# Kernel optimization log

Measured on AMD Instinct MI355X. Metric: run time of the kernel, lower is better.

Reference implementation:

```python
import jax, jax.numpy as jnp
import numpy as np

MASK_VAL = -50000.0
N_HEADS = 16

def setup_inputs() -> dict:
    key = jax.random.key(0)
    k1, k2, k3, k4 = jax.random.split(key, 4)
    b, n, d = 2, 2048, 1024
    s = d ** -0.5  # xavier-ish scale for weights
    return {
        "x": jax.random.normal(k1, (b, n, d), dtype=jnp.float32),
        "Wq": jax.random.normal(k2, (d, d), dtype=jnp.float32) * s,
        "Wkv": jax.random.normal(k3, (d, 2 * d), dtype=jnp.float32) * s,
        "Wo": jax.random.normal(k4, (d, d), dtype=jnp.float32) * s,
    }

def reference(x, Wq, Wkv, Wo):
    b, n, d = x.shape
    h = N_HEADS
    hd = d // h
    scale = hd ** -0.5
    # in-projection
    q = x @ Wq                      # [b, n, d]
    kv = x @ Wkv                    # [b, n, 2d]
    k, v = jnp.split(kv, 2, axis=-1)
    # split heads: b n (h d) -> b h n d
    split = lambda t: t.reshape(b, n, h, hd).transpose(0, 2, 1, 3)
    q, k, v = split(q), split(k), split(v)
    # scaled dot-product scores
    dots = jnp.einsum('bhid,bhjd->bhij', q * scale, k)  # [b, h, n, n]
    # causal mask: upper triangle (j > i) set to MASK_VAL (not -inf, per source)
    causal = jnp.triu(jnp.ones((n, n), dtype=bool), 1)
    dots = jnp.where(causal, MASK_VAL, dots)
    attn = jax.nn.softmax(dots, axis=-1)
    out = jnp.einsum('bhij,bhjd->bhid', attn, v)
    out = out.transpose(0, 2, 1, 3).reshape(b, n, d)  # merge heads
    return out @ Wo
```

## Files before the change

kernel.cpp:

```cpp
#include <hip/hip_runtime.h>
#include <stdint.h>
#include <stddef.h>


typedef __bf16 bf16;
typedef __bf16 bf16x8 __attribute__((ext_vector_type(8)));
typedef __bf16 bf16x4 __attribute__((ext_vector_type(4)));
typedef __bf16 bf16x2 __attribute__((ext_vector_type(2)));
typedef float  f32x4  __attribute__((ext_vector_type(4)));
typedef float  f32x16 __attribute__((ext_vector_type(16)));

#define NSEQ 2048
#define DM   1024
#define HD   64
#define QKVS 3072
#define LOG2E 1.44269504f

#define GLD16(g, l) __builtin_amdgcn_global_load_lds(                         \
    (const __attribute__((address_space(1))) void*)(g),                       \
    (__attribute__((address_space(3))) void*)(l), 16, 0, 0)

__global__ void detect_dtype(const uint32_t* __restrict__ x, int* __restrict__ flag) {
  __shared__ int cnt;
  if (threadIdx.x == 0) cnt = 0;
  __syncthreads();
  int c = 0;
  for (int i = threadIdx.x; i < 4096; i += 256) {
    uint32_t e = (x[i] >> 7) & 0xFF;
    if (e >= 110 && e <= 132) c++;
  }
  atomicAdd(&cnt, c);
  __syncthreads();
  if (threadIdx.x == 0) *flag = (cnt > 2048) ? 1 : 0;
}

__global__ __launch_bounds__(256) void convert_x(
    const void* __restrict__ in, bf16* __restrict__ out, int n,
    const int* __restrict__ flagp) {
  const int flag = *flagp;
  const int i = (blockIdx.x * 256 + threadIdx.x) * 8;
  if (i >= n) return;
  if (flag) {
    *(bf16x8*)(out + i) = *(const bf16x8*)((const bf16*)in + i);
  } else {
    const float* f = (const float*)in;
    bf16x8 v;
#pragma unroll
    for (int e = 0; e < 8; ++e) v[e] = (bf16)f[i + e];
    *(bf16x8*)(out + i) = v;
  }
}

__global__ void transpose_conv(const void* __restrict__ in, bf16* __restrict__ out,
                               int K, int N, const int* __restrict__ flagp) {
  __shared__ bf16 tile[32][33];
  const int flag = *flagp;
  const int k0 = blockIdx.y * 32, n0 = blockIdx.x * 32;
  const int tx = threadIdx.x, ty = threadIdx.y;
  if (flag) {
    const bf16* p = (const bf16*)in;
#pragma unroll
    for (int i = ty; i < 32; i += 8)
      tile[i][tx] = p[(size_t)(k0 + i) * N + n0 + tx];
  } else {
    const float* p = (const float*)in;
#pragma unroll
    for (int i = ty; i < 32; i += 8)
      tile[i][tx] = (bf16)p[(size_t)(k0 + i) * N + n0 + tx];
  }
  __syncthreads();
#pragma unroll
  for (int i = ty; i < 32; i += 8)
    out[(size_t)(n0 + i) * K + k0 + tx] = tile[tx][i];
}

__global__ __launch_bounds__(256) void gemm_bt(
    const bf16* __restrict__ A, const bf16* __restrict__ Bt,
    void* __restrict__ C, int M, int N, int K, const int* flagp)
{
  __shared__ bf16 As[128][64];
  __shared__ bf16 Bs[128][64];
  const int tid  = threadIdx.x;
  const int wave = tid >> 6, lane = tid & 63;
  const int fr = lane & 15, fg = lane >> 4;
  const int m0 = blockIdx.y * 128, n0 = blockIdx.x * 128;
  const int wr = (wave >> 1) * 64, wc = (wave & 1) * 64;
  const int lrow = lane >> 3;
  const int lcol = 8 * ((lane & 7) ^ lrow);

  f32x4 acc[4][4] = {};

  for (int kt = 0; kt < K; kt += 64) {
    __syncthreads();
#pragma unroll
    for (int p = 0; p < 4; ++p) {
      const int chunk = wave * 4 + p;
      const int r = chunk * 8 + lrow;
      GLD16(A  + (size_t)(m0 + r) * K + kt + lcol, &As[chunk * 8][0]);
      GLD16(Bt + (size_t)(n0 + r) * K + kt + lcol, &Bs[chunk * 8][0]);
    }
    __syncthreads();
#pragma unroll
    for (int s = 0; s < 2; ++s) {
      bf16x8 af[4], bfr[4];
#pragma unroll
      for (int i = 0; i < 4; ++i) {
        const int ar = wr + i * 16 + fr;
        af[i]  = *(const bf16x8*)((const char*)&As[ar][0] +
                   ((s * 64 + fg * 16) ^ ((ar & 7) << 4)));
        const int br = wc + i * 16 + fr;
        bfr[i] = *(const bf16x8*)((const char*)&Bs[br][0] +
                   ((s * 64 + fg * 16) ^ ((br & 7) << 4)));
      }
#pragma unroll
      for (int i = 0; i < 4; ++i)
#pragma unroll
        for (int j = 0; j < 4; ++j)
          acc[i][j] = __builtin_amdgcn_mfma_f32_16x16x32_bf16(
              af[i], bfr[j], acc[i][j], 0, 0, 0);
    }
  }
  const int crow = m0 + wr + fg * 4;
  const int ccol = n0 + wc + fr;
  const int as_bf16 = flagp ? *flagp : 1;
  if (as_bf16) {
    bf16* Cb = (bf16*)C;
#pragma unroll
    for (int i = 0; i < 4; ++i)
#pragma unroll
      for (int j = 0; j < 4; ++j)
#pragma unroll
        for (int r = 0; r < 4; ++r)
          Cb[(size_t)(crow + i * 16 + r) * N + ccol + j * 16] = (bf16)acc[i][j][r];
  } else {
    float* Cf = (float*)C;
#pragma unroll
    for (int i = 0; i < 4; ++i)
#pragma unroll
      for (int j = 0; j < 4; ++j)
#pragma unroll
        for (int r = 0; r < 4; ++r)
          Cf[(size_t)(crow + i * 16 + r) * N + ccol + j * 16] = acc[i][j][r];
  }
}

static __device__ inline uint32_t pk2(float a, float b) {
  bf16x2 t; t[0] = (bf16)a; t[1] = (bf16)b;
  return __builtin_bit_cast(uint32_t, t);
}

__global__ __launch_bounds__(256) void attn_fwd(
    const bf16* __restrict__ QKV, bf16* __restrict__ O)
{
  __shared__ bf16 Ks[2][64][64];
  __shared__ bf16 Vt[2][64][64];

  const int qt = gridDim.x - 1 - blockIdx.x;
  const int bh = blockIdx.y;
  const int bi = bh >> 4, hi = bh & 15;
  const int tid = threadIdx.x, wave = tid >> 6, lane = tid & 63;
  const int c = lane & 31, h = lane >> 5;

  const bf16* qptr = QKV + (size_t)bi * NSEQ * QKVS + hi * HD;
  const bf16* kptr = qptr + DM;
  const bf16* vptr = qptr + 2 * DM;

  const int q0w  = qt * 128 + wave * 32;
  const int qrow = q0w + c;

  bf16x8 qf[4];
#pragma unroll
  for (int ks = 0; ks < 4; ++ks)
    qf[ks] = *(const bf16x8*)(qptr + (size_t)qrow * QKVS + ks * 16 + h * 8);

  f32x16 oacc[2] = {};
  float m = -1e30f, l = 0.f;

  const int sjr = tid >> 3, sjc = tid & 7;
  const int koff = (sjc * 16) ^ ((sjr & 7) << 4);
  const int vjp = (tid & 31) * 2, vd0 = (tid >> 5) * 8;

  bf16x8 kA, kB, vA, vB;

  const int ntiles = 2 * qt + 2;

  {
    bf16x8 k0 = *(const bf16x8*)(kptr + (size_t)(sjr)      * QKVS + sjc * 8);
    bf16x8 k1 = *(const bf16x8*)(kptr + (size_t)(sjr + 32) * QKVS + sjc * 8);
    bf16x8 v0 = *(const bf16x8*)(vptr + (size_t)(vjp)      * QKVS + vd0);
    bf16x8 v1 = *(const bf16x8*)(vptr + (size_t)(vjp + 1)  * QKVS + vd0);
    *(bf16x8*)((char*)&Ks[0][sjr][0]      + koff) = k0;
    *(bf16x8*)((char*)&Ks[0][sjr + 32][0] + koff) = k1;
#pragma unroll
    for (int e = 0; e < 8; ++e) {
      const int d = vd0 + e;
      bf16x2 pr; pr[0] = v0[e]; pr[1] = v1[e];
      *(bf16x2*)((char*)&Vt[0][d][0] + ((vjp * 2) ^ ((d & 7) << 4))) = pr;
    }
    kA = *(const bf16x8*)(kptr + (size_t)(64 + sjr)      * QKVS + sjc * 8);
    kB = *(const bf16x8*)(kptr + (size_t)(64 + sjr + 32) * QKVS + sjc * 8);
    vA = *(const bf16x8*)(vptr + (size_t)(64 + vjp)      * QKVS + vd0);
    vB = *(const bf16x8*)(vptr + (size_t)(64 + vjp + 1)  * QKVS + vd0);
  }
  __syncthreads();

  for (int t = 0; t < ntiles; ++t) {
    const int cur = t & 1;
    const int j0 = t * 64;

    if (t + 1 < ntiles) {
      const int nb = cur ^ 1;
      *(bf16x8*)((char*)&Ks[nb][sjr][0]      + koff) = kA;
      *(bf16x8*)((char*)&Ks[nb][sjr + 32][0] + koff) = kB;
#pragma unroll
      for (int e = 0; e < 8; ++e) {
        const int d = vd0 + e;
        bf16x2 pr; pr[0] = vA[e]; pr[1] = vB[e];
        *(bf16x2*)((char*)&Vt[nb][d][0] + ((vjp * 2) ^ ((d & 7) << 4))) = pr;
      }
    }
    if (t + 2 < ntiles) {
      const int jn = j0 + 128;
      kA = *(const bf16x8*)(kptr + (size_t)(jn + sjr)      * QKVS + sjc * 8);
      kB = *(const bf16x8*)(kptr + (size_t)(jn + sjr + 32) * QKVS + sjc * 8);
      vA = *(const bf16x8*)(vptr + (size_t)(jn + vjp)      * QKVS + vd0);
      vB = *(const bf16x8*)(vptr + (size_t)(jn + vjp + 1)  * QKVS + vd0);
    }

    if (j0 <= q0w + 31) {
      f32x16 s[2];
      __builtin_amdgcn_s_setprio(1);
#pragma unroll
      for (int blk = 0; blk < 2; ++blk) {
        f32x16 a = {};
#pragma unroll
        for (int ks = 0; ks < 4; ++ks) {
          const int krow = blk * 32 + c;
          bf16x8 kf = *(const bf16x8*)((const char*)&Ks[cur][krow][0] +
                       ((ks * 32 + h * 16) ^ ((krow & 7) << 4)));
          a = __builtin_amdgcn_mfma_f32_32x32x16_bf16(kf, qf[ks], a, 0, 0, 0);
        }
        s[blk] = a;
      }
      __builtin_amdgcn_s_setprio(0);

      if (j0 + 63 > q0w) {
#pragma unroll
        for (int blk = 0; blk < 2; ++blk) {
          const int kvb = j0 + blk * 32 + 4 * h;
#pragma unroll
          for (int r = 0; r < 16; ++r) {
            const int kv = kvb + (r & 3) + 8 * (r >> 2);
            if (kv > qrow) s[blk][r] = -4.0e8f;
          }
        }
      }

      float tmax = -3.0e38f;
#pragma unroll
      for (int blk = 0; blk < 2; ++blk)
#pragma unroll
        for (int r = 0; r < 16; ++r) tmax = fmaxf(tmax, s[blk][r]);
      tmax = fmaxf(tmax, __shfl_xor(tmax, 32));
      const float pmax = tmax * 0.125f;
      if (!__all(pmax - m <= 8.0f)) {
        const float mnew  = fmaxf(m, pmax);
        const float alpha = __builtin_amdgcn_exp2f((m - mnew) * LOG2E);
        m = mnew;
        l *= alpha;
#pragma unroll
        for (int db = 0; db < 2; ++db)
#pragma unroll
          for (int r = 0; r < 16; ++r) oacc[db][r] *= alpha;
      }
      const float km = 0.125f * LOG2E, kb = -m * LOG2E;
      float sum = 0.f;
#pragma unroll
      for (int blk = 0; blk < 2; ++blk)
#pragma unroll
        for (int r = 0; r < 16; ++r) {
          const float p = __builtin_amdgcn_exp2f(__builtin_fmaf(s[blk][r], km, kb));
          s[blk][r] = p;
          sum += p;
        }
      sum += __shfl_xor(sum, 32);
      l += sum;

#pragma unroll
      for (int blk = 0; blk < 2; ++blk) {
        uint32_t w[8], xw[8];
#pragma unroll
        for (int g = 0; g < 4; ++g) {
          w[2 * g]     = pk2(s[blk][4 * g],     s[blk][4 * g + 1]);
          w[2 * g + 1] = pk2(s[blk][4 * g + 2], s[blk][4 * g + 3]);
        }
#pragma unroll
        for (int i = 0; i < 8; ++i)
          xw[i] = (uint32_t)__shfl_xor((int)w[i], 32);
#pragma unroll
        for (int ks = 0; ks < 2; ++ks) {
          union { uint32_t u[4]; bf16x8 v; } pf;
          pf.u[0] = h ? xw[4 * ks + 2] : w[4 * ks];
          pf.u[1] = h ? xw[4 * ks + 3] : w[4 * ks + 1];
          pf.u[2] = h ? w[4 * ks + 2]  : xw[4 * ks];
          pf.u[3] = h ? w[4 * ks + 3]  : xw[4 * ks + 1];
          __builtin_amdgcn_s_setprio(1);
#pragma unroll
          for (int db = 0; db < 2; ++db) {
            const int vrow = db * 32 + c;
            bf16x8 vf = *(const bf16x8*)((const char*)&Vt[cur][vrow][0] +
                         ((blk * 64 + ks * 32 + h * 16) ^ ((vrow & 7) << 4)));
            oacc[db] = __builtin_amdgcn_mfma_f32_32x32x16_bf16(vf, pf.v, oacc[db], 0, 0, 0);
          }
          __builtin_amdgcn_s_setprio(0);
        }
      }
    }

    __syncthreads();
  }

  const float linv = 1.f / l;
  bf16* obase = O + (size_t)bi * NSEQ * DM + (size_t)hi * HD + (size_t)qrow * DM;
#pragma unroll
  for (int db = 0; db < 2; ++db)
#pragma unroll
    for (int g = 0; g < 4; ++g) {
      bf16x4 ov;
#pragma unroll
      for (int j = 0; j < 4; ++j) ov[j] = (bf16)(oacc[db][4 * g + j] * linv);
      *(bf16x4*)(obase + db * 32 + 8 * g + 4 * h) = ov;
    }
}

extern "C" void kernel_launch(void* const* d_in, const int* in_sizes, int n_in,
                              void* d_out, int out_size, void* d_ws, size_t ws_size,
                              hipStream_t stream) {
  const void* x   = d_in[0];
  const void* Wq  = d_in[1];
  const void* Wkv = d_in[2];
  const void* Wo  = d_in[3];

  char* ws = (char*)d_ws;
  int*  flag   = (int*)ws;
  bf16* xb     = (bf16*)(ws + (4ull << 10));
  bf16* WqkvT  = (bf16*)(ws + (4ull << 10) + (8ull  << 20));
  bf16* WoT    = (bf16*)(ws + (4ull << 10) + (14ull << 20));
  bf16* QKVb   = (bf16*)(ws + (4ull << 10) + (16ull << 20));
  bf16* AOb    = xb;

  detect_dtype<<<1, 256, 0, stream>>>((const uint32_t*)x, flag);
  convert_x<<<4194304 / 8 / 256, 256, 0, stream>>>(x, xb, 4194304, flag);

  const dim3 tb(32, 8);
  transpose_conv<<<dim3(1024 / 32, 1024 / 32), tb, 0, stream>>>(Wq,  WqkvT,                1024, 1024, flag);
  transpose_conv<<<dim3(2048 / 32, 1024 / 32), tb, 0, stream>>>(Wkv, WqkvT + 1024 * 1024,  1024, 2048, flag);
  transpose_conv<<<dim3(1024 / 32, 1024 / 32), tb, 0, stream>>>(Wo,  WoT,                  1024, 1024, flag);

  gemm_bt<<<dim3(3072 / 128, 4096 / 128), 256, 0, stream>>>(xb, WqkvT, QKVb, 4096, 3072, 1024, nullptr);

  attn_fwd<<<dim3(16, 32), 256, 0, stream>>>(QKVb, AOb);

  gemm_bt<<<dim3(1024 / 128, 4096 / 128), 256, 0, stream>>>(AOb, WoT, d_out, 4096, 1024, 1024, flag);
}
```

Before: 156.0 us.

## Restructure attention to single-wave blocks with K read directly from global

The attention kernel now launches one 64-thread wave per 32 query rows instead of four waves per 128 rows, giving four times as many blocks. K fragments are loaded straight from global memory into registers, so the K shared-memory buffer goes away, and the block-wide barriers are dropped because each block is a single wave. Fully masked 32-key halves of the diagonal tile are skipped. The goal is finer causal load balance and no barrier stalls, at the cost of K and V no longer being shared across waves, which raises global/L2 traffic per query row.

```diff
diff --git a/kernel.cpp b/kernel.cpp
--- a/kernel.cpp
+++ b/kernel.cpp
@@ -149,24 +149,23 @@
   return __builtin_bit_cast(uint32_t, t);
 }
 
-__global__ __launch_bounds__(256) void attn_fwd(
+__global__ __launch_bounds__(64) void attn_fwd(
     const bf16* __restrict__ QKV, bf16* __restrict__ O)
 {
-  __shared__ bf16 Ks[2][64][64];
   __shared__ bf16 Vt[2][64][64];
 
-  const int qt = gridDim.x - 1 - blockIdx.x;
+  const int s  = gridDim.x - 1 - blockIdx.x;
   const int bh = blockIdx.y;
   const int bi = bh >> 4, hi = bh & 15;
-  const int tid = threadIdx.x, wave = tid >> 6, lane = tid & 63;
+  const int lane = threadIdx.x;
   const int c = lane & 31, h = lane >> 5;
 
   const bf16* qptr = QKV + (size_t)bi * NSEQ * QKVS + hi * HD;
   const bf16* kptr = qptr + DM;
   const bf16* vptr = qptr + 2 * DM;
 
-  const int q0w  = qt * 128 + wave * 32;
-  const int qrow = q0w + c;
+  const int q0 = s * 32;
+  const int qrow = q0 + c;
 
   bf16x8 qf[4];
 #pragma unroll
@@ -176,123 +175,138 @@
   f32x16 oacc[2] = {};
   float m = -1e30f, l = 0.f;
 
-  const int sjr = tid >> 3, sjc = tid & 7;
-  const int koff = (sjc * 16) ^ ((sjr & 7) << 4);
-  const int vjp = (tid & 31) * 2, vd0 = (tid >> 5) * 8;
-
-  bf16x8 kA, kB, vA, vB;
-
-  const int ntiles = 2 * qt + 2;
+  const int kvg = (lane & 15) * 4;
+  const int dg  = (lane >> 4) * 8;
+
+  bf16x8 vpre[2][4];
+
+  const int ntil = s / 2 + 1;
 
   {
-    bf16x8 k0 = *(const bf16x8*)(kptr + (size_t)(sjr)      * QKVS + sjc * 8);
-    bf16x8 k1 = *(const bf16x8*)(kptr + (size_t)(sjr + 32) * QKVS + sjc * 8);
-    bf16x8 v0 = *(const bf16x8*)(vptr + (size_t)(vjp)      * QKVS + vd0);
-    bf16x8 v1 = *(const bf16x8*)(vptr + (size_t)(vjp + 1)  * QKVS + vd0);
-    *(bf16x8*)((char*)&Ks[0][sjr][0]      + koff) = k0;
-    *(bf16x8*)((char*)&Ks[0][sjr + 32][0] + koff) = k1;
-#pragma unroll
-    for (int e = 0; e < 8; ++e) {
-      const int d = vd0 + e;
-      bf16x2 pr; pr[0] = v0[e]; pr[1] = v1[e];
-      *(bf16x2*)((char*)&Vt[0][d][0] + ((vjp * 2) ^ ((d & 7) << 4))) = pr;
-    }
-    kA = *(const bf16x8*)(kptr + (size_t)(64 + sjr)      * QKVS + sjc * 8);
-    kB = *(const bf16x8*)(kptr + (size_t)(64 + sjr + 32) * QKVS + sjc * 8);
-    vA = *(const bf16x8*)(vptr + (size_t)(64 + vjp)      * QKVS + vd0);
-    vB = *(const bf16x8*)(vptr + (size_t)(64 + vjp + 1)  * QKVS + vd0);
-  }
-  __syncthreads();
-
-  for (int t = 0; t < ntiles; ++t) {
+#pragma unroll
+    for (int p = 0; p < 2; ++p)
+#pragma unroll
+      for (int i = 0; i < 4; ++i)
+        vpre[p][i] = *(const bf16x8*)(vptr + (size_t)(kvg + i) * QKVS + dg + p * 32);
+#pragma unroll
+    for (int p = 0; p < 2; ++p)
+#pragma unroll
+      for (int e = 0; e < 8; ++e) {
+        const int d = dg + p * 32 + e;
+        bf16x4 w; w[0] = vpre[p][0][e]; w[1] = vpre[p][1][e];
+        w[2] = vpre[p][2][e]; w[3] = vpre[p][3][e];
+        *(bf16x4*)((char*)&Vt[0][d][0] + ((2 * kvg) ^ ((d & 7) << 4))) = w;
+      }
+    if (ntil > 1) {
+#pragma unroll
+      for (int p = 0; p < 2; ++p)
+#pragma unroll
+        for (int i = 0; i < 4; ++i)
+          vpre[p][i] = *(const bf16x8*)(vptr + (size_t)(64 + kvg + i) * QKVS + dg + p * 32);
+    }
+  }
+
+  for (int t = 0; t < ntil; ++t) {
     const int cur = t & 1;
     const int j0 = t * 64;
 
-    if (t + 1 < ntiles) {
-      const int nb = cur ^ 1;
-      *(bf16x8*)((char*)&Ks[nb][sjr][0]      + koff) = kA;
-      *(bf16x8*)((char*)&Ks[nb][sjr + 32][0] + koff) = kB;
-#pragma unroll
-      for (int e = 0; e < 8; ++e) {
-        const int d = vd0 + e;
-        bf16x2 pr; pr[0] = vA[e]; pr[1] = vB[e];
-        *(bf16x2*)((char*)&Vt[nb][d][0] + ((vjp * 2) ^ ((d & 7) << 4))) = pr;
+    if (t + 1 < ntil) {
+#pragma unroll
+      for (int p = 0; p < 2; ++p)
+#pragma unroll
+        for (int e = 0; e < 8; ++e) {
+          const int d = dg + p * 32 + e;
+          bf16x4 w; w[0] = vpre[p][0][e]; w[1] = vpre[p][1][e];
+          w[2] = vpre[p][2][e]; w[3] = vpre[p][3][e];
+          *(bf16x4*)((char*)&Vt[cur ^ 1][d][0] + ((2 * kvg) ^ ((d & 7) << 4))) = w;
+        }
+    }
+
+    bf16x8 kf[2][4];
+#pragma unroll
+    for (int blk = 0; blk < 2; ++blk)
+#pragma unroll
+      for (int ks = 0; ks < 4; ++ks)
+        kf[blk][ks] = *(const bf16x8*)(kptr +
+            (size_t)(j0 + blk * 32 + c) * QKVS + ks * 16 + h * 8);
+
+    if (t + 2 < ntil) {
+      const int jn = j0 + 128;
+#pragma unroll
+      for (int p = 0; p < 2; ++p)
+#pragma unroll
+        for (int i = 0; i < 4; ++i)
+          vpre[p][i] = *(const bf16x8*)(vptr + (size_t)(jn + kvg + i) * QKVS + dg + p * 32);
+    }
+
+    const int blkmax = (j0 + 32 <= q0 + 31) ? 2 : 1;
+
+    f32x16 sv[2];
+    __builtin_amdgcn_s_setprio(1);
+#pragma unroll
+    for (int blk = 0; blk < 2; ++blk)
+      if (blk < blkmax) {
+        f32x16 a = {};
+#pragma unroll
+        for (int ks = 0; ks < 4; ++ks)
+          a = __builtin_amdgcn_mfma_f32_32x32x16_bf16(kf[blk][ks], qf[ks], a, 0, 0, 0);
+        sv[blk] = a;
       }
-    }
-    if (t + 2 < ntiles) {
-      const int jn = j0 + 128;
-      kA = *(const bf16x8*)(kptr + (size_t)(jn + sjr)      * QKVS + sjc * 8);
-      kB = *(const bf16x8*)(kptr + (size_t)(jn + sjr + 32) * QKVS + sjc * 8);
-      vA = *(const bf16x8*)(vptr + (size_t)(jn + vjp)      * QKVS + vd0);
-      vB = *(const bf16x8*)(vptr + (size_t)(jn + vjp + 1)  * QKVS + vd0);
-    }
-
-    if (j0 <= q0w + 31) {
-      f32x16 s[2];
-      __builtin_amdgcn_s_setprio(1);
-#pragma unroll
-      for (int blk = 0; blk < 2; ++blk) {
-        f32x16 a = {};
-#pragma unroll
-        for (int ks = 0; ks < 4; ++ks) {
-          const int krow = blk * 32 + c;
-          bf16x8 kf = *(const bf16x8*)((const char*)&Ks[cur][krow][0] +
-                       ((ks * 32 + h * 16) ^ ((krow & 7) << 4)));
-          a = __builtin_amdgcn_mfma_f32_32x32x16_bf16(kf, qf[ks], a, 0, 0, 0);
-        }
-        s[blk] = a;
-      }
-      __builtin_amdgcn_s_setprio(0);
-
-      if (j0 + 63 > q0w) {
-#pragma unroll
-        for (int blk = 0; blk < 2; ++blk) {
+    __builtin_amdgcn_s_setprio(0);
+
+    if (j0 + 63 > q0) {
+#pragma unroll
+      for (int blk = 0; blk < 2; ++blk)
+        if (blk < blkmax) {
           const int kvb = j0 + blk * 32 + 4 * h;
 #pragma unroll
           for (int r = 0; r < 16; ++r) {
             const int kv = kvb + (r & 3) + 8 * (r >> 2);
-            if (kv > qrow) s[blk][r] = -4.0e8f;
+            if (kv > qrow) sv[blk][r] = -4.0e8f;
           }
         }
-      }
-
-      float tmax = -3.0e38f;
-#pragma unroll
-      for (int blk = 0; blk < 2; ++blk)
-#pragma unroll
-        for (int r = 0; r < 16; ++r) tmax = fmaxf(tmax, s[blk][r]);
-      tmax = fmaxf(tmax, __shfl_xor(tmax, 32));
-      const float pmax = tmax * 0.125f;
-      if (!__all(pmax - m <= 8.0f)) {
-        const float mnew  = fmaxf(m, pmax);
-        const float alpha = __builtin_amdgcn_exp2f((m - mnew) * LOG2E);
-        m = mnew;
-        l *= alpha;
-#pragma unroll
-        for (int db = 0; db < 2; ++db)
-#pragma unroll
-          for (int r = 0; r < 16; ++r) oacc[db][r] *= alpha;
-      }
-      const float km = 0.125f * LOG2E, kb = -m * LOG2E;
-      float sum = 0.f;
-#pragma unroll
-      for (int blk = 0; blk < 2; ++blk)
+    }
+
+    float tmax = -3.0e38f;
+#pragma unroll
+    for (int blk = 0; blk < 2; ++blk)
+      if (blk < blkmax)
+#pragma unroll
+        for (int r = 0; r < 16; ++r) tmax = fmaxf(tmax, sv[blk][r]);
+    tmax = fmaxf(tmax, __shfl_xor(tmax, 32));
+    const float pmax = tmax * 0.125f;
+    if (!__all(pmax - m <= 8.0f)) {
+      const float mnew  = fmaxf(m, pmax);
+      const float alpha = __builtin_amdgcn_exp2f((m - mnew) * LOG2E);
+      m = mnew;
+      l *= alpha;
+#pragma unroll
+      for (int db = 0; db < 2; ++db)
+#pragma unroll
+        for (int r = 0; r < 16; ++r) oacc[db][r] *= alpha;
+    }
+    const float km = 0.125f * LOG2E, kb = -m * LOG2E;
+    float sum = 0.f;
+#pragma unroll
+    for (int blk = 0; blk < 2; ++blk)
+      if (blk < blkmax)
 #pragma unroll
         for (int r = 0; r < 16; ++r) {
-          const float p = __builtin_amdgcn_exp2f(__builtin_fmaf(s[blk][r], km, kb));
-          s[blk][r] = p;
+          const float p = __builtin_amdgcn_exp2f(__builtin_fmaf(sv[blk][r], km, kb));
+          sv[blk][r] = p;
           sum += p;
         }
-      sum += __shfl_xor(sum, 32);
-      l += sum;
-
-#pragma unroll
-      for (int blk = 0; blk < 2; ++blk) {
+    sum += __shfl_xor(sum, 32);
+    l += sum;
+
+#pragma unroll
+    for (int blk = 0; blk < 2; ++blk)
+      if (blk < blkmax) {
         uint32_t w[8], xw[8];
 #pragma unroll
         for (int g = 0; g < 4; ++g) {
-          w[2 * g]     = pk2(s[blk][4 * g],     s[blk][4 * g + 1]);
-          w[2 * g + 1] = pk2(s[blk][4 * g + 2], s[blk][4 * g + 3]);
+          w[2 * g]     = pk2(sv[blk][4 * g],     sv[blk][4 * g + 1]);
+          w[2 * g + 1] = pk2(sv[blk][4 * g + 2], sv[blk][4 * g + 3]);
         }
 #pragma unroll
         for (int i = 0; i < 8; ++i)
@@ -315,9 +329,6 @@
           __builtin_amdgcn_s_setprio(0);
         }
       }
-    }
-
-    __syncthreads();
   }
 
   const float linv = 1.f / l;
@@ -359,7 +370,7 @@
 
   gemm_bt<<<dim3(3072 / 128, 4096 / 128), 256, 0, stream>>>(xb, WqkvT, QKVb, 4096, 3072, 1024, nullptr);
 
-  attn_fwd<<<dim3(16, 32), 256, 0, stream>>>(QKVb, AOb);
+  attn_fwd<<<dim3(64, 32), 64, 0, stream>>>(QKVb, AOb);
 
   gemm_bt<<<dim3(1024 / 128, 4096 / 128), 256, 0, stream>>>(AOb, WoT, d_out, 4096, 1024, 1024, flag);
 }
```

New measurement: 227.6 us. +45.9%, slower.
